# Optimization experiments

Hardware: AMD Instinct MI355X
Metric: run time of the kernel (lower is better)

The kernel has to match this reference:

```python
import jax, jax.numpy as jnp
import numpy as np

N_ROWS, N_COLS = 4, 4
EPS = 1e-5


def setup_inputs() -> dict:
    key = jax.random.key(0)
    ks = jax.random.split(key, 4)
    x = jax.random.normal(ks[0], (32, 32, 256, 256), dtype=jnp.float32)
    gamma = jnp.ones((32,), dtype=jnp.float32)
    beta = jnp.zeros((32,), dtype=jnp.float32)
    prelu_a = jnp.full((1,), 0.25, dtype=jnp.float32)  # torch PReLU default init
    conv_w = jax.random.normal(ks[1], (32, 32, 3, 3), dtype=jnp.float32) * (1.0 / np.sqrt(32 * 9))
    conv_b = jax.random.normal(ks[2], (32,), dtype=jnp.float32) * 0.01
    return {"x": x, "gamma": gamma, "beta": beta, "prelu_a": prelu_a,
            "conv_w": conv_w, "conv_b": conv_b}


def reference(x, gamma, beta, prelu_a, conv_w, conv_b):
    B, C, H, W = x.shape
    rh, rw = H // N_ROWS, W // N_COLS
    # Fold the region grid into a leading region axis: [R, B, C, rh, rw]
    xr = x.reshape(B, C, N_ROWS, rh, N_COLS, rw)
    xr = xr.transpose(2, 4, 0, 1, 3, 5).reshape(N_ROWS * N_COLS, B, C, rh, rw)
    # BatchNorm (training mode): per-region, per-channel stats over (B, rh, rw)
    mean = xr.mean(axis=(1, 3, 4), keepdims=True)
    var = jnp.mean((xr - mean) ** 2, axis=(1, 3, 4), keepdims=True)  # biased var
    g = gamma[None, None, :, None, None]
    b = beta[None, None, :, None, None]
    y = (xr - mean) * jax.lax.rsqrt(var + EPS) * g + b
    # PReLU with a single shared slope
    y = jnp.where(y > 0, y, prelu_a[0] * y)
    # Conv2d 3x3 pad=1 applied per region (zero padding at region borders)
    yb = y.reshape(N_ROWS * N_COLS * B, C, rh, rw)
    out = jax.lax.conv_general_dilated(
        yb, conv_w, window_strides=(1, 1), padding=((1, 1), (1, 1)),
        dimension_numbers=("NCHW", "OIHW", "NCHW"))
    out = out + conv_b[None, :, None, None]
    # Reassemble region grid -> full image
    out = out.reshape(N_ROWS, N_COLS, B, C, rh, rw)
    out = out.transpose(2, 3, 0, 4, 1, 5).reshape(B, C, H, W)
    return out
```

## Files before the change

### kernel.cpp

```cpp
#include <hip/hip_runtime.h>
#include <hip/hip_bf16.h>


#define EPS 1e-5f

typedef float f32x4 __attribute__((ext_vector_type(4)));
typedef __bf16 bf16x8 __attribute__((ext_vector_type(8)));
typedef short short8 __attribute__((ext_vector_type(8)));

__device__ inline short f2bf(float f) {
  union { __hip_bfloat16 h; short s; } u;
  u.h = __float2bfloat16(f);
  return u.s;
}

__global__ __launch_bounds__(256) void stats_partial(
    const float* __restrict__ x, float* __restrict__ ws_sum,
    float* __restrict__ ws_sq) {
  int plane = blockIdx.x;
  const float* base = x + (size_t)plane * 65536;
  int t = threadIdx.x;
  float s[4] = {0.f, 0.f, 0.f, 0.f}, q[4] = {0.f, 0.f, 0.f, 0.f};
#pragma unroll
  for (int R = 0; R < 4; ++R) {
#pragma unroll
    for (int ii = 0; ii < 16; ++ii) {
      int idx4 = (R * 16 + ii) * 256 + t;
      float4 v = *reinterpret_cast<const float4*>(base + (size_t)idx4 * 4);
      s[R] += (v.x + v.y) + (v.z + v.w);
      q[R] += (v.x * v.x + v.y * v.y) + (v.z * v.z + v.w * v.w);
    }
  }
#pragma unroll
  for (int R = 0; R < 4; ++R) {
#pragma unroll
    for (int off = 8; off; off >>= 1) {
      s[R] += __shfl_down(s[R], off);
      q[R] += __shfl_down(q[R], off);
    }
  }
  __shared__ float red[2][4][4][4];
  int lane = t & 63, wv = t >> 6;
  if ((lane & 15) == 0) {
    int Cc = lane >> 4;
#pragma unroll
    for (int R = 0; R < 4; ++R) {
      red[0][wv][Cc][R] = s[R];
      red[1][wv][Cc][R] = q[R];
    }
  }
  __syncthreads();
  if (t < 16) {
    int R = t >> 2, Cc = t & 3;
    float S = 0.f, Q = 0.f;
#pragma unroll
    for (int w = 0; w < 4; ++w) {
      S += red[0][w][Cc][R];
      Q += red[1][w][Cc][R];
    }
    ws_sum[plane * 16 + t] = S;
    ws_sq[plane * 16 + t] = Q;
  }
}

__global__ __launch_bounds__(256) void weights_prep(
    const float* __restrict__ conv_w, unsigned short* __restrict__ wfrag) {
  int idx = blockIdx.x * 256 + threadIdx.x;
  if (idx >= 18 * 64) return;
  int lane = idx & 63;
  int th = idx >> 6;
  int t = th >> 1, h = th & 1;
  int dy = t / 3, dx = t - dy * 3;
  int oc = h * 16 + (lane & 15);
  int ic0 = (lane >> 4) * 8;
#pragma unroll
  for (int j = 0; j < 8; ++j) {
    float w = conv_w[((oc * 32 + ic0 + j) * 3 + dy) * 3 + dx];
    wfrag[(size_t)idx * 8 + j] = (unsigned short)f2bf(w);
  }
}

__global__ __launch_bounds__(256) void conv_mfma(
    const float* __restrict__ x, const unsigned short* __restrict__ wfrag,
    const float* __restrict__ conv_b, const float* __restrict__ prelu_a,
    const float* __restrict__ ws_sum, const float* __restrict__ ws_sq,
    const float* __restrict__ gamma, const float* __restrict__ beta,
    float* __restrict__ out) {
  __shared__ short lds_y[10 * 64 * 32];

  int blk0 = blockIdx.x;
  int blk = (blk0 & 7) * 512 + (blk0 >> 3);
  int rt = blk & 7;
  int p = (blk >> 3) & 15;
  int b = blk >> 7;
  int R = p >> 2, Cc = p & 3;
  int h0 = rt * 8;
  int tid = threadIdx.x;
  int lane = tid & 63;
  float pa = prelu_a[0];

  float* abuf = (float*)lds_y;
  if (tid < 32) {
    int c = tid;
    float S = 0.f, Q = 0.f;
#pragma unroll
    for (int bb = 0; bb < 32; ++bb) {
      int idx = (bb * 32 + c) * 16 + p;
      S += ws_sum[idx];
      Q += ws_sq[idx];
    }
    const float inv = 1.0f / 131072.0f;
    float mean = S * inv;
    float var = Q * inv - mean * mean;
    float rstd = rsqrtf(var + EPS);
    float a = rstd * gamma[c];
    abuf[c] = a;
    abuf[32 + c] = beta[c] - mean * a;
  }
  __syncthreads();

  int s = (tid >> 4) & 3;
  int c4 = tid & 15;
  int srb = tid >> 6;
  int ic0 = s * 8;

  float a_r[8], b_r[8];
#pragma unroll
  for (int j = 0; j < 8; ++j) {
    a_r[j] = abuf[ic0 + j];
    b_r[j] = abuf[32 + ic0 + j];
  }
  __syncthreads();

  auto stage_load = [&](f32x4(&vv)[8], int sr) {
    int lr = h0 - 1 + sr;
#pragma unroll
    for (int kk = 0; kk < 8; ++kk) vv[kk] = f32x4{0.f, 0.f, 0.f, 0.f};
    if ((unsigned)lr < 64u) {
      const float* xp =
          x + (((size_t)(b * 32 + ic0) * 256 + R * 64 + lr) * 256) + Cc * 64 +
          c4 * 4;
#pragma unroll
      for (int kk = 0; kk < 8; ++kk)
        vv[kk] = *reinterpret_cast<const f32x4*>(xp + (size_t)kk * 65536);
    }
  };
  auto stage_write = [&](const f32x4(&vv)[8], int sr) {
#pragma unroll
    for (int j = 0; j < 4; ++j) {
      short8 pk;
#pragma unroll
      for (int kk = 0; kk < 8; ++kk) {
        float e = fmaf(a_r[kk], vv[kk][j], b_r[kk]);
        e = e > 0.f ? e : pa * e;
        pk[kk] = f2bf(e);
      }
      int colp = c4 * 4 + ((j + c4) & 3);
      int slot = (s + (colp >> 1)) & 3;
      *reinterpret_cast<short8*>(&lds_y[(sr * 64 + colp) * 32 + slot * 8]) = pk;
    }
  };

  {
    f32x4 va[8], vb[8], vc[8];
    stage_load(va, srb);
    stage_load(vb, srb + 4);
    stage_write(va, srb);
    if (tid < 128) stage_load(vc, srb + 8);
    stage_write(vb, srb + 4);
    if (tid < 128) stage_write(vc, srb + 8);
  }
  __syncthreads();

  bf16x8 wf[18];
#pragma unroll
  for (int th = 0; th < 18; ++th) {
    short8 sv =
        *reinterpret_cast<const short8*>(wfrag + ((size_t)th * 64 + lane) * 8);
    wf[th] = __builtin_bit_cast(bf16x8, sv);
  }
  int l15 = lane & 15, l4 = lane >> 4;
  f32x4 bias0, bias1;
#pragma unroll
  for (int i = 0; i < 4; ++i) {
    bias0[i] = conv_b[l4 * 4 + i];
    bias1[i] = conv_b[16 + l4 * 4 + i];
  }

  int wv = tid >> 6;
  const short8 z8 = {0, 0, 0, 0, 0, 0, 0, 0};
  for (int g = 0; g < 8; ++g) {
    int gi = wv * 8 + g;
    int r = gi >> 2;
    int c0 = (gi & 3) * 16;
    f32x4 acc0 = bias0, acc1 = bias1;
#pragma unroll
    for (int t9 = 0; t9 < 9; ++t9) {
      const int dy = t9 / 3, dx = t9 - dy * 3;
      int sr = r + dy;
      int col_in = c0 + l15 + dx - 1;
      int colc = col_in & 63;
      int colp = (colc & ~3) | ((colc + (colc >> 2)) & 3);
      int slot = (l4 + (colp >> 1)) & 3;
      short8 sv = *reinterpret_cast<const short8*>(
          &lds_y[(sr * 64 + colp) * 32 + slot * 8]);
      if (dx == 0) {
        if (c0 == 0 && l15 == 0) sv = z8;
      }
      if (dx == 2) {
        if (c0 == 48 && l15 == 15) sv = z8;
      }
      bf16x8 bv = __builtin_bit_cast(bf16x8, sv);
      acc0 = __builtin_amdgcn_mfma_f32_16x16x32_bf16(wf[t9 * 2], bv, acc0, 0, 0, 0);
      acc1 = __builtin_amdgcn_mfma_f32_16x16x32_bf16(wf[t9 * 2 + 1], bv, acc1, 0, 0, 0);
    }
    int grow = R * 64 + h0 + r;
    int gcol = Cc * 64 + c0 + l15;
    float* ob = out + (size_t)b * 2097152 + (size_t)grow * 256 + gcol;
#pragma unroll
    for (int i = 0; i < 4; ++i) {
      __builtin_nontemporal_store(acc0[i], &ob[(size_t)(l4 * 4 + i) * 65536]);
      __builtin_nontemporal_store(acc1[i],
                                  &ob[(size_t)(16 + l4 * 4 + i) * 65536]);
    }
  }
}

extern "C" void kernel_launch(void* const* d_in, const int* in_sizes, int n_in,
                              void* d_out, int out_size, void* d_ws,
                              size_t ws_size, hipStream_t stream) {
  const float* x = (const float*)d_in[0];
  const float* gamma = (const float*)d_in[1];
  const float* beta = (const float*)d_in[2];
  const float* prelu_a = (const float*)d_in[3];
  const float* conv_w = (const float*)d_in[4];
  const float* conv_b = (const float*)d_in[5];
  float* out = (float*)d_out;

  float* ws = (float*)d_ws;
  float* ws_sum = ws;
  float* ws_sq = ws + 16384;
  unsigned short* wfrag = (unsigned short*)(ws + 32768);

  weights_prep<<<5, 256, 0, stream>>>(conv_w, wfrag);
  stats_partial<<<1024, 256, 0, stream>>>(x, ws_sum, ws_sq);
  conv_mfma<<<4096, 256, 0, stream>>>(x, wfrag, conv_b, prelu_a, ws_sum, ws_sq,
                                      gamma, beta, out);
}
```

Measured before the change: 165.8 us.

## Fuse weight prep into stats kernel, transpose stats layout, prefetch inputs early

Folds the weight-fragment prep into the stats kernel as extra blocks, removing one kernel launch. The partial-sum workspace is transposed to [region][channel][batch], so each conv block reads its per-channel sums contiguously instead of with a 16-float stride. The conv kernel now issues its first two global input loads before the stats reduction and barrier, so load latency overlaps with that reduction. The cost is more registers held live across the barrier, which may lower occupancy.

```diff
diff --git a/kernel.cpp b/kernel.cpp
--- a/kernel.cpp
+++ b/kernel.cpp
@@ -14,12 +14,34 @@
   return u.s;
 }
 
-__global__ __launch_bounds__(256) void stats_partial(
+__global__ __launch_bounds__(256) void stats_prep(
     const float* __restrict__ x, float* __restrict__ ws_sum,
-    float* __restrict__ ws_sq) {
-  int plane = blockIdx.x;
+    float* __restrict__ ws_sq, const float* __restrict__ conv_w,
+    unsigned short* __restrict__ wfrag) {
+  int blk = blockIdx.x;
+  int t = threadIdx.x;
+
+  if (blk >= 1024) {
+    int idx = (blk - 1024) * 256 + t;
+    if (idx < 18 * 64) {
+      int lane = idx & 63;
+      int th = idx >> 6;
+      int tt = th >> 1, h = th & 1;
+      int dy = tt / 3, dx = tt - dy * 3;
+      int oc = h * 16 + (lane & 15);
+      int ic0 = (lane >> 4) * 8;
+#pragma unroll
+      for (int j = 0; j < 8; ++j) {
+        float w = conv_w[((oc * 32 + ic0 + j) * 3 + dy) * 3 + dx];
+        wfrag[(size_t)idx * 8 + j] = (unsigned short)f2bf(w);
+      }
+    }
+    return;
+  }
+
+  int plane = blk;
+  int b = plane >> 5, c = plane & 31;
   const float* base = x + (size_t)plane * 65536;
-  int t = threadIdx.x;
   float s[4] = {0.f, 0.f, 0.f, 0.f}, q[4] = {0.f, 0.f, 0.f, 0.f};
 #pragma unroll
   for (int R = 0; R < 4; ++R) {
@@ -58,25 +80,8 @@
       S += red[0][w][Cc][R];
       Q += red[1][w][Cc][R];
     }
-    ws_sum[plane * 16 + t] = S;
-    ws_sq[plane * 16 + t] = Q;
-  }
-}
-
-__global__ __launch_bounds__(256) void weights_prep(
-    const float* __restrict__ conv_w, unsigned short* __restrict__ wfrag) {
-  int idx = blockIdx.x * 256 + threadIdx.x;
-  if (idx >= 18 * 64) return;
-  int lane = idx & 63;
-  int th = idx >> 6;
-  int t = th >> 1, h = th & 1;
-  int dy = t / 3, dx = t - dy * 3;
-  int oc = h * 16 + (lane & 15);
-  int ic0 = (lane >> 4) * 8;
-#pragma unroll
-  for (int j = 0; j < 8; ++j) {
-    float w = conv_w[((oc * 32 + ic0 + j) * 3 + dy) * 3 + dx];
-    wfrag[(size_t)idx * 8 + j] = (unsigned short)f2bf(w);
+    ws_sum[(t * 32 + c) * 32 + b] = S;
+    ws_sq[(t * 32 + c) * 32 + b] = Q;
   }
 }
 
@@ -99,15 +104,39 @@
   int lane = tid & 63;
   float pa = prelu_a[0];
 
+  int s = (tid >> 4) & 3;
+  int c4 = tid & 15;
+  int srb = tid >> 6;
+  int ic0 = s * 8;
+
+  auto stage_load = [&](f32x4(&vv)[8], int sr) {
+    int lr = h0 - 1 + sr;
+#pragma unroll
+    for (int kk = 0; kk < 8; ++kk) vv[kk] = f32x4{0.f, 0.f, 0.f, 0.f};
+    if ((unsigned)lr < 64u) {
+      const float* xp =
+          x + (((size_t)(b * 32 + ic0) * 256 + R * 64 + lr) * 256) + Cc * 64 +
+          c4 * 4;
+#pragma unroll
+      for (int kk = 0; kk < 8; ++kk)
+        vv[kk] = *reinterpret_cast<const f32x4*>(xp + (size_t)kk * 65536);
+    }
+  };
+
+  f32x4 va[8], vb[8];
+  stage_load(va, srb);
+  stage_load(vb, srb + 4);
+
   float* abuf = (float*)lds_y;
   if (tid < 32) {
     int c = tid;
+    const float* su = ws_sum + (p * 32 + c) * 32;
+    const float* sq = ws_sq + (p * 32 + c) * 32;
     float S = 0.f, Q = 0.f;
 #pragma unroll
     for (int bb = 0; bb < 32; ++bb) {
-      int idx = (bb * 32 + c) * 16 + p;
-      S += ws_sum[idx];
-      Q += ws_sq[idx];
+      S += su[bb];
+      Q += sq[bb];
     }
     const float inv = 1.0f / 131072.0f;
     float mean = S * inv;
@@ -119,11 +148,6 @@
   }
   __syncthreads();
 
-  int s = (tid >> 4) & 3;
-  int c4 = tid & 15;
-  int srb = tid >> 6;
-  int ic0 = s * 8;
-
   float a_r[8], b_r[8];
 #pragma unroll
   for (int j = 0; j < 8; ++j) {
@@ -132,19 +156,6 @@
   }
   __syncthreads();
 
-  auto stage_load = [&](f32x4(&vv)[8], int sr) {
-    int lr = h0 - 1 + sr;
-#pragma unroll
-    for (int kk = 0; kk < 8; ++kk) vv[kk] = f32x4{0.f, 0.f, 0.f, 0.f};
-    if ((unsigned)lr < 64u) {
-      const float* xp =
-          x + (((size_t)(b * 32 + ic0) * 256 + R * 64 + lr) * 256) + Cc * 64 +
-          c4 * 4;
-#pragma unroll
-      for (int kk = 0; kk < 8; ++kk)
-        vv[kk] = *reinterpret_cast<const f32x4*>(xp + (size_t)kk * 65536);
-    }
-  };
   auto stage_write = [&](const f32x4(&vv)[8], int sr) {
 #pragma unroll
     for (int j = 0; j < 4; ++j) {
@@ -162,9 +173,7 @@
   };
 
   {
-    f32x4 va[8], vb[8], vc[8];
-    stage_load(va, srb);
-    stage_load(vb, srb + 4);
+    f32x4 vc[8];
     stage_write(va, srb);
     if (tid < 128) stage_load(vc, srb + 8);
     stage_write(vb, srb + 4);
@@ -242,8 +251,7 @@
   float* ws_sq = ws + 16384;
   unsigned short* wfrag = (unsigned short*)(ws + 32768);
 
-  weights_prep<<<5, 256, 0, stream>>>(conv_w, wfrag);
-  stats_partial<<<1024, 256, 0, stream>>>(x, ws_sum, ws_sq);
+  stats_prep<<<1029, 256, 0, stream>>>(x, ws_sum, ws_sq, conv_w, wfrag);
   conv_mfma<<<4096, 256, 0, stream>>>(x, wfrag, conv_b, prelu_a, ws_sum, ws_sq,
                                       gamma, beta, out);
 }
```

Result: faster. 160.7 us (-3.1%).
